# Kernel optimization log

Hardware: AMD Instinct MI355X
Metric: run time of the kernel (lower is better)

## Reference

```python
import jax, jax.numpy as jnp
import numpy as np

N_NODES = 50000
N_EDGES = 800000
NUM_FEATURES = 128
HIDDEN = 128


def _gcn_conv(x, src, dst, norm, W, b, num_nodes):
    # x: [N, F_in], W: [F_in, F_out]
    h = x @ W                              # dense transform first (PyG order)
    msg = h[src] * norm[:, None]           # gather + per-edge scale
    out = jax.ops.segment_sum(msg, dst, num_segments=num_nodes)  # scatter-add
    return out + b


def _prep_edges(edge_index, num_nodes):
    # add self loops
    loop = jnp.arange(num_nodes, dtype=edge_index.dtype)
    src = jnp.concatenate([edge_index[0], loop])
    dst = jnp.concatenate([edge_index[1], loop])
    # symmetric normalization deg^{-1/2}[src] * deg^{-1/2}[dst]
    deg = jax.ops.segment_sum(jnp.ones_like(dst, dtype=jnp.float32), dst,
                              num_segments=num_nodes)
    dinv = jnp.where(deg > 0, jax.lax.rsqrt(deg), 0.0)
    norm = dinv[src] * dinv[dst]
    return src, dst, norm


def setup_inputs() -> dict:
    key = jax.random.key(0)
    ks = jax.random.split(key, 5)
    s1 = 1.0 / np.sqrt(NUM_FEATURES)
    s2 = 1.0 / np.sqrt(HIDDEN)
    return {
        "x": jax.random.normal(ks[0], (N_NODES, NUM_FEATURES), jnp.float32),
        "edge_index": jax.random.randint(ks[1], (2, N_EDGES), 0, N_NODES,
                                         dtype=jnp.int64),
        "W1": jax.random.normal(ks[2], (NUM_FEATURES, HIDDEN), jnp.float32) * s1,
        "b1": jnp.zeros((HIDDEN,), jnp.float32),
        "W2": jax.random.normal(ks[3], (HIDDEN, HIDDEN), jnp.float32) * s2,
        "b2": jnp.zeros((HIDDEN,), jnp.float32),
        "Wout": jax.random.normal(ks[4], (HIDDEN, 1), jnp.float32) * s2,
        "bout": jnp.zeros((1,), jnp.float32),
    }


def reference(x, edge_index, W1, b1, W2, b2, Wout, bout):
    num_nodes = x.shape[0]
    src, dst, norm = _prep_edges(edge_index, num_nodes)
    h = _gcn_conv(x, src, dst, norm, W1, b1, num_nodes)
    h = jax.nn.relu(h)
    h = _gcn_conv(h, src, dst, norm, W2, b2, num_nodes)
    h = jax.nn.relu(h)
    return jax.nn.sigmoid(h @ Wout + bout)
```

## Files before the change

### kernel.cpp

```cpp
#include <hip/hip_runtime.h>
#include <math.h>

#define NN 50000
#define NE 800000
#define NBUK 196
#define PBLK 256
#define EPB (NE / PBLK)

typedef __attribute__((ext_vector_type(8))) short bf16x8;
typedef __attribute__((ext_vector_type(4))) float f32x4;

__device__ __forceinline__ unsigned short f2b(float f) {
  union { float f; unsigned u; } v; v.f = f;
  unsigned r = v.u + 0x7FFF + ((v.u >> 16) & 1);
  return (unsigned short)(r >> 16);
}
__device__ __forceinline__ float plo(unsigned v) {
  union { unsigned u; float f; } t; t.u = v << 16; return t.f;
}
__device__ __forceinline__ float phi(unsigned v) {
  union { unsigned u; float f; } t; t.u = v & 0xFFFF0000u; return t.f;
}

__device__ __forceinline__ int edge_val(const void* ei, long long idx, int is64) {
  if (is64) return (int)((const long long*)ei)[idx];
  return ((const int*)ei)[idx];
}

__global__ __launch_bounds__(256) void k_phist(const void* __restrict__ ei,
                                               int* __restrict__ bh,
                                               const float* __restrict__ W1,
                                               const float* __restrict__ W2,
                                               unsigned short* __restrict__ Wt1,
                                               unsigned short* __restrict__ Wt2) {
  if (threadIdx.x < 128) {
    int gi = blockIdx.x * 128 + threadIdx.x;
    int sel = gi >> 14;
    int j = gi & 16383;
    int k = j >> 7, n = j & 127;
    (sel ? Wt2 : Wt1)[n * 128 + k] = f2b((sel ? W2 : W1)[j]);
  }
  __shared__ int hist[NBUK];
  __shared__ int sflag;
  if (threadIdx.x < 64) {
    unsigned v = ((const unsigned*)ei)[2 * threadIdx.x + 1];
    unsigned long long m = __ballot(v == 0u);
    if (threadIdx.x == 0) sflag = (m == ~0ull) ? 1 : 0;
  }
  if (threadIdx.x < NBUK) hist[threadIdx.x] = 0;
  __syncthreads();
  int is64 = sflag;
  int base = blockIdx.x * EPB;
  for (int e = base + threadIdx.x; e < base + EPB; e += 256) {
    int d = edge_val(ei, (long long)NE + e, is64);
    atomicAdd(&hist[d >> 8], 1);
  }
  __syncthreads();
  if (threadIdx.x < NBUK) bh[threadIdx.x * PBLK + blockIdx.x] = hist[threadIdx.x];
}

__global__ __launch_bounds__(256) void k_pscanA(int* __restrict__ bh,
                                                int* __restrict__ colsum) {
  __shared__ int sh[256];
  int k = blockIdx.x, t = threadIdx.x;
  int v = bh[k * PBLK + t];
  sh[t] = v;
  __syncthreads();
  for (int s = 1; s < 256; s <<= 1) {
    int u = (t >= s) ? sh[t - s] : 0;
    __syncthreads();
    sh[t] += u;
    __syncthreads();
  }
  bh[k * PBLK + t] = sh[t] - v;
  if (t == 255) colsum[k] = sh[255];
}

__global__ __launch_bounds__(256) void k_pscanB(const int* __restrict__ colsum,
                                                int* __restrict__ bstart) {
  __shared__ int sh[256];
  int t = threadIdx.x;
  sh[t] = (t < NBUK) ? colsum[t] : 0;
  __syncthreads();
  for (int s = 1; s < 256; s <<= 1) {
    int u = (t >= s) ? sh[t - s] : 0;
    __syncthreads();
    sh[t] += u;
    __syncthreads();
  }
  if (t <= NBUK) bstart[t] = (t == 0) ? 0 : sh[t - 1];
}

__global__ __launch_bounds__(256) void k_pscat(const void* __restrict__ ei,
                                               const int* __restrict__ bh,
                                               const int* __restrict__ bstart,
                                               unsigned* __restrict__ epk) {
  __shared__ int cur[NBUK];
  __shared__ int sflag;
  if (threadIdx.x < 64) {
    unsigned v = ((const unsigned*)ei)[2 * threadIdx.x + 1];
    unsigned long long m = __ballot(v == 0u);
    if (threadIdx.x == 0) sflag = (m == ~0ull) ? 1 : 0;
  }
  if (threadIdx.x < NBUK)
    cur[threadIdx.x] = bstart[threadIdx.x] + bh[threadIdx.x * PBLK + blockIdx.x];
  __syncthreads();
  int is64 = sflag;
  int base = blockIdx.x * EPB;
  for (int e = base + threadIdx.x; e < base + EPB; e += 256) {
    int d = edge_val(ei, (long long)NE + e, is64);
    int s = edge_val(ei, e, is64);
    int p = atomicAdd(&cur[d >> 8], 1);
    epk[p] = (unsigned)s | ((unsigned)(d & 255) << 16);
  }
}

__global__ __launch_bounds__(256) void k_bofffill(const unsigned* __restrict__ epk,
                                                  const int* __restrict__ bstart,
                                                  int* __restrict__ off,
                                                  float* __restrict__ dinv,
                                                  unsigned short* __restrict__ csr16) {
  __shared__ int hist[256];
  __shared__ int cur[256];
  int k = blockIdx.x, t = threadIdx.x;
  hist[t] = 0;
  __syncthreads();
  int e0 = bstart[k], e1 = bstart[k + 1];
  for (int e = e0 + t; e < e1; e += 256)
    atomicAdd(&hist[(epk[e] >> 16) & 255], 1);
  __syncthreads();
  int myc = hist[t];
  for (int s = 1; s < 256; s <<= 1) {
    int u = (t >= s) ? hist[t - s] : 0;
    __syncthreads();
    hist[t] += u;
    __syncthreads();
  }
  int excl = hist[t] - myc;
  int node = k * 256 + t;
  if (node < NN) {
    off[node] = e0 + excl;
    dinv[node] = rsqrtf((float)(myc + 1));
  }
  cur[t] = e0 + excl;
  __syncthreads();
  for (int e = e0 + t; e < e1; e += 256) {
    unsigned pk = epk[e];
    int p = atomicAdd(&cur[(pk >> 16) & 255], 1);
    csr16[p] = (unsigned short)(pk & 0xFFFFu);
  }
  if (k == 0 && t == 0) off[NN] = NE;
}

template <int A_F32>
__global__ __launch_bounds__(256, 2) void k_mgemm(const void* __restrict__ Ap,
                                                  const unsigned short* __restrict__ Wt,
                                                  const float* __restrict__ dinv,
                                                  unsigned short* __restrict__ Out,
                                                  int M) {
  int wid  = (blockIdx.x * blockDim.x + threadIdx.x) >> 6;
  int lane = threadIdx.x & 63;
  int nw   = (gridDim.x * blockDim.x) >> 6;
  int r  = lane & 15;
  int kg = lane >> 4;
  bf16x8 wf[8][4];
#pragma unroll
  for (int n = 0; n < 8; ++n)
#pragma unroll
    for (int kk = 0; kk < 4; ++kk)
      wf[n][kk] = *(const bf16x8*)&Wt[(n * 16 + r) * 128 + kk * 32 + kg * 8];
  int nstr = M >> 4;
  for (int s = wid; s < nstr; s += nw) {
    int row = s * 16 + r;
    bf16x8 xf[4];
    if (A_F32) {
      const float* Ar = (const float*)Ap + (long long)row * 128 + kg * 8;
#pragma unroll
      for (int kk = 0; kk < 4; ++kk) {
        float4 lo4 = *(const float4*)(Ar + kk * 32);
        float4 hi4 = *(const float4*)(Ar + kk * 32 + 4);
        bf16x8 t;
        t[0] = (short)f2b(lo4.x); t[1] = (short)f2b(lo4.y);
        t[2] = (short)f2b(lo4.z); t[3] = (short)f2b(lo4.w);
        t[4] = (short)f2b(hi4.x); t[5] = (short)f2b(hi4.y);
        t[6] = (short)f2b(hi4.z); t[7] = (short)f2b(hi4.w);
        xf[kk] = t;
      }
    } else {
      const unsigned short* Ar = (const unsigned short*)Ap + (long long)row * 128 + kg * 8;
#pragma unroll
      for (int kk = 0; kk < 4; ++kk)
        xf[kk] = *(const bf16x8*)(Ar + kk * 32);
    }
    f32x4 acc[8];
#pragma unroll
    for (int n = 0; n < 8; ++n) acc[n] = (f32x4){0.f, 0.f, 0.f, 0.f};
#pragma unroll
    for (int kk = 0; kk < 4; ++kk)
#pragma unroll
      for (int n = 0; n < 8; ++n)
        acc[n] = __builtin_amdgcn_mfma_f32_16x16x32_bf16(wf[n][kk], xf[kk], acc[n], 0, 0, 0);
    float dv = dinv[row];
    unsigned short* Or = Out + (long long)row * 128 + kg * 4;
#pragma unroll
    for (int n = 0; n < 8; ++n) {
      uint2 o;
      o.x = (unsigned)f2b(acc[n][0] * dv) | ((unsigned)f2b(acc[n][1] * dv) << 16);
      o.y = (unsigned)f2b(acc[n][2] * dv) | ((unsigned)f2b(acc[n][3] * dv) << 16);
      *(uint2*)(Or + n * 16) = o;
    }
  }
}

template <int FINAL>
__global__ __launch_bounds__(256) void k_agg(const unsigned short* __restrict__ Tb,
                                             const int* __restrict__ off,
                                             const unsigned short* __restrict__ csr16,
                                             const float* __restrict__ dinv,
                                             const float* __restrict__ bias,
                                             const float* __restrict__ wout,
                                             const float* __restrict__ bout,
                                             void* __restrict__ outp) {
  const uint4* Tw4 = (const uint4*)Tb;
  int wid  = (blockIdx.x * blockDim.x + threadIdx.x) >> 6;
  int lane = threadIdx.x & 63;
  int grp  = lane >> 4;
  int li   = lane & 15;
  int nw   = (gridDim.x * blockDim.x) >> 6;
  float4 bA = ((const float4*)bias)[li * 2];
  float4 bB = ((const float4*)bias)[li * 2 + 1];
  float4 wA = make_float4(0.f, 0.f, 0.f, 0.f), wB = wA;
  if (FINAL) { wA = ((const float4*)wout)[li * 2]; wB = ((const float4*)wout)[li * 2 + 1]; }
  for (int d = wid; d < NN; d += nw) {
    int e0 = off[d], e1 = off[d + 1];
    int ne = e1 - e0;
    int np = ne >> 2, rem = ne & 3;
    int s_init = (grp == 0) ? d : ((grp - 1) < rem ? (int)csr16[e1 - 1 - (grp - 1)] : -1);
    float a0 = 0.f, a1 = 0.f, a2 = 0.f, a3 = 0.f, a4 = 0.f, a5 = 0.f, a6 = 0.f, a7 = 0.f;
    if (s_init >= 0) {
      uint4 v = Tw4[s_init * 16 + li];
      a0 = plo(v.x); a1 = phi(v.x); a2 = plo(v.y); a3 = phi(v.y);
      a4 = plo(v.z); a5 = phi(v.z); a6 = plo(v.w); a7 = phi(v.w);
    }
    int base = e0 + grp;
    int st = 0;
    for (; st + 4 <= np; st += 4) {
      int s0 = csr16[base + 4 * st];
      int s1 = csr16[base + 4 * st + 4];
      int s2 = csr16[base + 4 * st + 8];
      int s3 = csr16[base + 4 * st + 12];
      uint4 v0 = Tw4[s0 * 16 + li];
      uint4 v1 = Tw4[s1 * 16 + li];
      uint4 v2 = Tw4[s2 * 16 + li];
      uint4 v3 = Tw4[s3 * 16 + li];
      a0 += plo(v0.x); a1 += phi(v0.x); a2 += plo(v0.y); a3 += phi(v0.y);
      a4 += plo(v0.z); a5 += phi(v0.z); a6 += plo(v0.w); a7 += phi(v0.w);
      a0 += plo(v1.x); a1 += phi(v1.x); a2 += plo(v1.y); a3 += phi(v1.y);
      a4 += plo(v1.z); a5 += phi(v1.z); a6 += plo(v1.w); a7 += phi(v1.w);
      a0 += plo(v2.x); a1 += phi(v2.x); a2 += plo(v2.y); a3 += phi(v2.y);
      a4 += plo(v2.z); a5 += phi(v2.z); a6 += plo(v2.w); a7 += phi(v2.w);
      a0 += plo(v3.x); a1 += phi(v3.x); a2 += plo(v3.y); a3 += phi(v3.y);
      a4 += plo(v3.z); a5 += phi(v3.z); a6 += plo(v3.w); a7 += phi(v3.w);
    }
    for (; st < np; ++st) {
      int s = csr16[base + 4 * st];
      uint4 v = Tw4[s * 16 + li];
      a0 += plo(v.x); a1 += phi(v.x); a2 += plo(v.y); a3 += phi(v.y);
      a4 += plo(v.z); a5 += phi(v.z); a6 += plo(v.w); a7 += phi(v.w);
    }
    a0 += __shfl_xor(a0, 16, 64); a1 += __shfl_xor(a1, 16, 64);
    a2 += __shfl_xor(a2, 16, 64); a3 += __shfl_xor(a3, 16, 64);
    a4 += __shfl_xor(a4, 16, 64); a5 += __shfl_xor(a5, 16, 64);
    a6 += __shfl_xor(a6, 16, 64); a7 += __shfl_xor(a7, 16, 64);
    a0 += __shfl_xor(a0, 32, 64); a1 += __shfl_xor(a1, 32, 64);
    a2 += __shfl_xor(a2, 32, 64); a3 += __shfl_xor(a3, 32, 64);
    a4 += __shfl_xor(a4, 32, 64); a5 += __shfl_xor(a5, 32, 64);
    a6 += __shfl_xor(a6, 32, 64); a7 += __shfl_xor(a7, 32, 64);
    float dv = dinv[d];
    a0 = fmaxf(fmaf(a0, dv, bA.x), 0.f);
    a1 = fmaxf(fmaf(a1, dv, bA.y), 0.f);
    a2 = fmaxf(fmaf(a2, dv, bA.z), 0.f);
    a3 = fmaxf(fmaf(a3, dv, bA.w), 0.f);
    a4 = fmaxf(fmaf(a4, dv, bB.x), 0.f);
    a5 = fmaxf(fmaf(a5, dv, bB.y), 0.f);
    a6 = fmaxf(fmaf(a6, dv, bB.z), 0.f);
    a7 = fmaxf(fmaf(a7, dv, bB.w), 0.f);
    if (FINAL) {
      float r = a0 * wA.x + a1 * wA.y + a2 * wA.z + a3 * wA.w
              + a4 * wB.x + a5 * wB.y + a6 * wB.z + a7 * wB.w;
      r += __shfl_xor(r, 8, 64);
      r += __shfl_xor(r, 4, 64);
      r += __shfl_xor(r, 2, 64);
      r += __shfl_xor(r, 1, 64);
      if (lane == 0) ((float*)outp)[d] = 1.f / (1.f + __expf(-(r + bout[0])));
    } else if (grp == 0) {
      uint4 o;
      o.x = (unsigned)f2b(a0) | ((unsigned)f2b(a1) << 16);
      o.y = (unsigned)f2b(a2) | ((unsigned)f2b(a3) << 16);
      o.z = (unsigned)f2b(a4) | ((unsigned)f2b(a5) << 16);
      o.w = (unsigned)f2b(a6) | ((unsigned)f2b(a7) << 16);
      ((uint4*)outp)[d * 16 + li] = o;
    }
  }
}

extern "C" void kernel_launch(void* const* d_in, const int* in_sizes, int n_in,
                              void* d_out, int out_size, void* d_ws, size_t ws_size,
                              hipStream_t stream) {
  const float* x  = (const float*)d_in[0];
  const void*  ei = d_in[1];
  const float* W1 = (const float*)d_in[2];
  const float* b1 = (const float*)d_in[3];
  const float* W2 = (const float*)d_in[4];
  const float* b2 = (const float*)d_in[5];
  const float* Wo = (const float*)d_in[6];
  const float* bo = (const float*)d_in[7];
  float* out = (float*)d_out;

  char* p = (char*)d_ws;
  auto alloc = [&](size_t bytes) {
    char* r = p;
    p += (bytes + 511) & ~(size_t)511;
    return r;
  };
  int*   bh     = (int*)alloc(sizeof(int) * NBUK * PBLK);
  int*   colsum = (int*)alloc(sizeof(int) * NBUK);
  int*   bstart = (int*)alloc(sizeof(int) * (NBUK + 1));
  int*   off    = (int*)alloc(sizeof(int) * (NN + 1));
  float* dinv   = (float*)alloc(sizeof(float) * NN);
  unsigned short* csr16 = (unsigned short*)alloc(sizeof(short) * NE);
  unsigned short* Wt1 = (unsigned short*)alloc(sizeof(short) * 128 * 128);
  unsigned short* Wt2 = (unsigned short*)alloc(sizeof(short) * 128 * 128);
  unsigned short* T   = (unsigned short*)alloc(sizeof(short) * (size_t)NN * 128);
  unsigned short* H   = (unsigned short*)alloc(sizeof(short) * (size_t)NN * 128);
  unsigned* epk = (unsigned*)T;

  k_phist<<<PBLK, 256, 0, stream>>>(ei, bh, W1, W2, Wt1, Wt2);
  k_pscanA<<<NBUK, 256, 0, stream>>>(bh, colsum);
  k_pscanB<<<1, 256, 0, stream>>>(colsum, bstart);
  k_pscat<<<PBLK, 256, 0, stream>>>(ei, bh, bstart, epk);
  k_bofffill<<<NBUK, 256, 0, stream>>>(epk, bstart, off, dinv, csr16);

  k_mgemm<1><<<512, 256, 0, stream>>>(x, Wt1, dinv, T, NN);
  k_agg<0><<<2048, 256, 0, stream>>>(T, off, csr16, dinv, b1, nullptr, nullptr, H);
  k_mgemm<0><<<512, 256, 0, stream>>>(H, Wt2, dinv, T, NN);
  k_agg<1><<<2048, 256, 0, stream>>>(T, off, csr16, dinv, b2, Wo, bo, out);
}
```

Before: 216.7 us.

## Split feature columns into four quarter-planes mapped per XCD in aggregation

Stores the transformed features as four 32-column planes, each [NN][32], instead of row-major [NN][128]. Each aggregation block is tied to one plane chosen by blockIdx mod 8, so blocks that share a plane run on the same XCD pair and that plane's working set can stay in their local L2. Each wave now handles one node, with 16 edge groups of 4 lanes, and partial results are reduced through shuffles. The final layer writes per-quarter partial dot products, and a new small kernel sums them and applies the sigmoid. The cost is four times as many edge-index reads and one extra launch, and the XCD mapping assumes round-robin block dispatch.

```diff
diff --git a/kernel.cpp b/kernel.cpp
--- a/kernel.cpp
+++ b/kernel.cpp
@@ -187,10 +187,10 @@
         xf[kk] = t;
       }
     } else {
-      const unsigned short* Ar = (const unsigned short*)Ap + (long long)row * 128 + kg * 8;
+      const unsigned short* Ar = (const unsigned short*)Ap;
 #pragma unroll
       for (int kk = 0; kk < 4; ++kk)
-        xf[kk] = *(const bf16x8*)(Ar + kk * 32);
+        xf[kk] = *(const bf16x8*)(Ar + ((size_t)(kk * NN + row) * 32) + kg * 8);
     }
     f32x4 acc[8];
 #pragma unroll
@@ -201,13 +201,14 @@
       for (int n = 0; n < 8; ++n)
         acc[n] = __builtin_amdgcn_mfma_f32_16x16x32_bf16(wf[n][kk], xf[kk], acc[n], 0, 0, 0);
     float dv = dinv[row];
-    unsigned short* Or = Out + (long long)row * 128 + kg * 4;
 #pragma unroll
     for (int n = 0; n < 8; ++n) {
+      int q = n >> 1;
+      unsigned short* Or = Out + ((size_t)(q * NN + row) * 32) + (n & 1) * 16 + kg * 4;
       uint2 o;
       o.x = (unsigned)f2b(acc[n][0] * dv) | ((unsigned)f2b(acc[n][1] * dv) << 16);
       o.y = (unsigned)f2b(acc[n][2] * dv) | ((unsigned)f2b(acc[n][3] * dv) << 16);
-      *(uint2*)(Or + n * 16) = o;
+      *(uint2*)Or = o;
     }
   }
 }
@@ -219,55 +220,49 @@
                                              const float* __restrict__ dinv,
                                              const float* __restrict__ bias,
                                              const float* __restrict__ wout,
-                                             const float* __restrict__ bout,
                                              void* __restrict__ outp) {
-  const uint4* Tw4 = (const uint4*)Tb;
-  int wid  = (blockIdx.x * blockDim.x + threadIdx.x) >> 6;
+  const uint4* Tw = (const uint4*)Tb;
+  int bid  = blockIdx.x;
+  int xcd  = bid & 7;
+  int q    = xcd >> 1;
+  int wb   = (bid >> 3) * 2 + (xcd & 1);
+  int wave = threadIdx.x >> 6;
   int lane = threadIdx.x & 63;
-  int grp  = lane >> 4;
-  int li   = lane & 15;
-  int nw   = (gridDim.x * blockDim.x) >> 6;
-  float4 bA = ((const float4*)bias)[li * 2];
-  float4 bB = ((const float4*)bias)[li * 2 + 1];
+  int g    = lane >> 2;
+  int li   = lane & 3;
+  float4 bA = ((const float4*)bias)[q * 8 + li * 2];
+  float4 bB = ((const float4*)bias)[q * 8 + li * 2 + 1];
   float4 wA = make_float4(0.f, 0.f, 0.f, 0.f), wB = wA;
-  if (FINAL) { wA = ((const float4*)wout)[li * 2]; wB = ((const float4*)wout)[li * 2 + 1]; }
-  for (int d = wid; d < NN; d += nw) {
+  if (FINAL) {
+    wA = ((const float4*)wout)[q * 8 + li * 2];
+    wB = ((const float4*)wout)[q * 8 + li * 2 + 1];
+  }
+  const size_t qbase = (size_t)q * NN;
+  for (int d = wb * 4 + wave; d < NN; d += 2048) {
     int e0 = off[d], e1 = off[d + 1];
     int ne = e1 - e0;
-    int np = ne >> 2, rem = ne & 3;
-    int s_init = (grp == 0) ? d : ((grp - 1) < rem ? (int)csr16[e1 - 1 - (grp - 1)] : -1);
+    int np = ne >> 4, rem = ne & 15;
+    int s_init = (g == 0) ? d : ((g - 1) < rem ? (int)csr16[e1 - 1 - (g - 1)] : -1);
     float a0 = 0.f, a1 = 0.f, a2 = 0.f, a3 = 0.f, a4 = 0.f, a5 = 0.f, a6 = 0.f, a7 = 0.f;
     if (s_init >= 0) {
-      uint4 v = Tw4[s_init * 16 + li];
+      uint4 v = Tw[(qbase + s_init) * 4 + li];
       a0 = plo(v.x); a1 = phi(v.x); a2 = plo(v.y); a3 = phi(v.y);
       a4 = plo(v.z); a5 = phi(v.z); a6 = plo(v.w); a7 = phi(v.w);
     }
-    int base = e0 + grp;
-    int st = 0;
-    for (; st + 4 <= np; st += 4) {
-      int s0 = csr16[base + 4 * st];
-      int s1 = csr16[base + 4 * st + 4];
-      int s2 = csr16[base + 4 * st + 8];
-      int s3 = csr16[base + 4 * st + 12];
-      uint4 v0 = Tw4[s0 * 16 + li];
-      uint4 v1 = Tw4[s1 * 16 + li];
-      uint4 v2 = Tw4[s2 * 16 + li];
-      uint4 v3 = Tw4[s3 * 16 + li];
-      a0 += plo(v0.x); a1 += phi(v0.x); a2 += plo(v0.y); a3 += phi(v0.y);
-      a4 += plo(v0.z); a5 += phi(v0.z); a6 += plo(v0.w); a7 += phi(v0.w);
-      a0 += plo(v1.x); a1 += phi(v1.x); a2 += plo(v1.y); a3 += phi(v1.y);
-      a4 += plo(v1.z); a5 += phi(v1.z); a6 += plo(v1.w); a7 += phi(v1.w);
-      a0 += plo(v2.x); a1 += phi(v2.x); a2 += plo(v2.y); a3 += phi(v2.y);
-      a4 += plo(v2.z); a5 += phi(v2.z); a6 += plo(v2.w); a7 += phi(v2.w);
-      a0 += plo(v3.x); a1 += phi(v3.x); a2 += plo(v3.y); a3 += phi(v3.y);
-      a4 += plo(v3.z); a5 += phi(v3.z); a6 += plo(v3.w); a7 += phi(v3.w);
-    }
-    for (; st < np; ++st) {
-      int s = csr16[base + 4 * st];
-      uint4 v = Tw4[s * 16 + li];
+    for (int st = 0; st < np; ++st) {
+      int s = (int)__builtin_nontemporal_load(&csr16[e0 + 16 * st + g]);
+      uint4 v = Tw[(qbase + s) * 4 + li];
       a0 += plo(v.x); a1 += phi(v.x); a2 += plo(v.y); a3 += phi(v.y);
       a4 += plo(v.z); a5 += phi(v.z); a6 += plo(v.w); a7 += phi(v.w);
     }
+    a0 += __shfl_xor(a0, 4, 64);  a1 += __shfl_xor(a1, 4, 64);
+    a2 += __shfl_xor(a2, 4, 64);  a3 += __shfl_xor(a3, 4, 64);
+    a4 += __shfl_xor(a4, 4, 64);  a5 += __shfl_xor(a5, 4, 64);
+    a6 += __shfl_xor(a6, 4, 64);  a7 += __shfl_xor(a7, 4, 64);
+    a0 += __shfl_xor(a0, 8, 64);  a1 += __shfl_xor(a1, 8, 64);
+    a2 += __shfl_xor(a2, 8, 64);  a3 += __shfl_xor(a3, 8, 64);
+    a4 += __shfl_xor(a4, 8, 64);  a5 += __shfl_xor(a5, 8, 64);
+    a6 += __shfl_xor(a6, 8, 64);  a7 += __shfl_xor(a7, 8, 64);
     a0 += __shfl_xor(a0, 16, 64); a1 += __shfl_xor(a1, 16, 64);
     a2 += __shfl_xor(a2, 16, 64); a3 += __shfl_xor(a3, 16, 64);
     a4 += __shfl_xor(a4, 16, 64); a5 += __shfl_xor(a5, 16, 64);
@@ -288,20 +283,27 @@
     if (FINAL) {
       float r = a0 * wA.x + a1 * wA.y + a2 * wA.z + a3 * wA.w
               + a4 * wB.x + a5 * wB.y + a6 * wB.z + a7 * wB.w;
-      r += __shfl_xor(r, 8, 64);
-      r += __shfl_xor(r, 4, 64);
+      r += __shfl_xor(r, 1, 64);
       r += __shfl_xor(r, 2, 64);
-      r += __shfl_xor(r, 1, 64);
-      if (lane == 0) ((float*)outp)[d] = 1.f / (1.f + __expf(-(r + bout[0])));
-    } else if (grp == 0) {
+      if (lane == 0) ((float*)outp)[qbase + d] = r;
+    } else if (g == 0) {
       uint4 o;
       o.x = (unsigned)f2b(a0) | ((unsigned)f2b(a1) << 16);
       o.y = (unsigned)f2b(a2) | ((unsigned)f2b(a3) << 16);
       o.z = (unsigned)f2b(a4) | ((unsigned)f2b(a5) << 16);
       o.w = (unsigned)f2b(a6) | ((unsigned)f2b(a7) << 16);
-      ((uint4*)outp)[d * 16 + li] = o;
-    }
-  }
+      ((uint4*)outp)[(qbase + d) * 4 + li] = o;
+    }
+  }
+}
+
+__global__ __launch_bounds__(256) void k_fin(const float* __restrict__ part,
+                                             const float* __restrict__ bout,
+                                             float* __restrict__ out) {
+  int i = blockIdx.x * 256 + threadIdx.x;
+  if (i >= NN) return;
+  float r = part[i] + part[NN + i] + part[2 * NN + i] + part[3 * NN + i] + bout[0];
+  out[i] = 1.f / (1.f + __expf(-r));
 }
 
 extern "C" void kernel_launch(void* const* d_in, const int* in_sizes, int n_in,
@@ -333,6 +335,7 @@
   unsigned short* Wt2 = (unsigned short*)alloc(sizeof(short) * 128 * 128);
   unsigned short* T   = (unsigned short*)alloc(sizeof(short) * (size_t)NN * 128);
   unsigned short* H   = (unsigned short*)alloc(sizeof(short) * (size_t)NN * 128);
+  float* part = (float*)alloc(sizeof(float) * 4 * NN);
   unsigned* epk = (unsigned*)T;
 
   k_phist<<<PBLK, 256, 0, stream>>>(ei, bh, W1, W2, Wt1, Wt2);
@@ -342,7 +345,8 @@
   k_bofffill<<<NBUK, 256, 0, stream>>>(epk, bstart, off, dinv, csr16);
 
   k_mgemm<1><<<512, 256, 0, stream>>>(x, Wt1, dinv, T, NN);
-  k_agg<0><<<2048, 256, 0, stream>>>(T, off, csr16, dinv, b1, nullptr, nullptr, H);
+  k_agg<0><<<2048, 256, 0, stream>>>(T, off, csr16, dinv, b1, nullptr, H);
   k_mgemm<0><<<512, 256, 0, stream>>>(H, Wt2, dinv, T, NN);
-  k_agg<1><<<2048, 256, 0, stream>>>(T, off, csr16, dinv, b2, Wo, bo, out);
-}
+  k_agg<1><<<2048, 256, 0, stream>>>(T, off, csr16, dinv, b2, Wo, part);
+  k_fin<<<(NN + 255) / 256, 256, 0, stream>>>(part, bo, out);
+}
```

After: 312.0 us. 44.0% more time.
